# Kernel optimization log

Hardware: AMD Instinct MI355X
Metric: run time of the kernel (lower is better)

The kernel has to match this reference:

```python
import math
import jax, jax.numpy as jnp
import numpy as np

LEVELS = 4          # wavelet_levels
PRUNE = 0.05        # wavelet_packet_prune_ratio
EPS = 1e-6
SQRT2 = math.sqrt(2.0)


def _haar_split(c):
    n = c.shape[-1]
    if n % 2 != 0:
        c = jnp.concatenate([c, jnp.zeros(c.shape[:-1] + (1,), c.dtype)], axis=-1)
    even, odd = c[..., 0::2], c[..., 1::2]
    return (even + odd) / SQRT2, (even - odd) / SQRT2, n


def _haar_merge(low, high, orig):
    even = (low + high) / SQRT2
    odd = (low - high) / SQRT2
    out = jnp.stack([even, odd], axis=-1).reshape(*low.shape[:-1], low.shape[-1] * 2)
    return out[..., :orig]


def _coherence(c, gpu):
    unit = c / jnp.maximum(jnp.abs(c), EPS)
    return jnp.clip(jnp.abs(jnp.mean(unit * jnp.conj(gpu), axis=-1, keepdims=True)), 0.0, 1.0)


def _cost(c, gpu):
    # gauge-aware packet cost: Shannon entropy of energy distribution + (1 - coherence)
    if c.shape[-1] <= 1:
        return jnp.float32(0.0)
    e = jnp.square(jnp.abs(c))
    p = jnp.maximum(e / jnp.maximum(e.sum(-1, keepdims=True), EPS), EPS)
    ent = -(p * jnp.log(p)).sum(-1)
    coh = _coherence(c, gpu)[..., 0]
    return jax.lax.stop_gradient(jnp.mean(ent + (1.0 - coh)))


def _band_center(path):
    if not path:
        return 0.0
    idx = 0
    for b in path:
        idx = (idx << 1) | b
    return (idx + 0.5) / (2 ** len(path))


def _leaf_gain(c, path, depth, gpu, Wp, bp, Wo, bo, lfg, sigma, hfg, cutoff):
    mag = jnp.maximum(jnp.abs(c), EPS)
    phase = jnp.arctan2(c.imag, c.real) / math.pi
    nle = jnp.broadcast_to(
        jnp.log(jnp.maximum(jnp.mean(jnp.square(jnp.abs(c)), -1, keepdims=True), EPS)), mag.shape)
    dn = jnp.full(mag.shape, depth / max(1, LEVELS), mag.dtype)
    bcv = _band_center(path)
    bc = jnp.full(mag.shape, bcv, mag.dtype)
    coh = jnp.broadcast_to(_coherence(c, gpu), mag.shape)
    pos = jnp.broadcast_to(jnp.linspace(0.0, 1.0, c.shape[-1], dtype=mag.dtype), mag.shape)
    feats = jnp.stack([jnp.log(mag), phase, nle, dn, bc, coh, pos], axis=-1)  # [..., n, 7]
    gd = jax.nn.silu(feats @ Wp.T + bp) @ Wo.T + bo                            # [..., n, 2]
    dm = 0.25 * jnp.tanh(gd[..., 0])
    dp = 0.5 * math.pi * jnp.tanh(gd[..., 1])
    lbb = 1.0 + lfg * jnp.exp(-(bcv * bcv) / jnp.square(sigma))
    hbd = hfg + (1.0 - hfg) * jax.nn.sigmoid((cutoff - bcv) / sigma)
    gm = lbb * hbd * (1.0 + lfg * coh) * (hfg + (1.0 - hfg) * coh) * jnp.exp(dm)
    return jax.lax.complex(gm * jnp.cos(dp), gm * jnp.sin(dp))  # torch.polar


def _filter_leaf(c, path, depth, total_e, gpu, params):
    Wp, bp, Wo, bo, lfg, sigma, hfg, cutoff = params
    node_e = jax.lax.stop_gradient(jnp.square(jnp.abs(c)).sum())
    filtered = c * _leaf_gain(c, path, depth, gpu, Wp, bp, Wo, bo, lfg, sigma, hfg, cutoff)
    coh_v = jax.lax.stop_gradient(jnp.mean(_coherence(c, gpu)))
    # spectral subtraction
    fm = jnp.abs(filtered)
    nf = jnp.median(fm, axis=-1, keepdims=True)
    damping = hfg + (1.0 - hfg) * jax.nn.sigmoid((cutoff - _band_center(path)) / sigma)
    den = jax.nn.relu(fm - (1.0 - damping) * nf)
    filtered = den * (filtered / jnp.maximum(fm, EPS))
    # prune low-energy / low-coherence leaves
    prune = jnp.logical_or(node_e / total_e < PRUNE, coh_v < PRUNE)
    return jnp.where(prune, filtered * jnp.square(hfg), filtered)


def _apply_node(c, depth, path, total_e, gpu, params):
    cost = _cost(c, gpu)
    leaf = _filter_leaf(c, path, depth, total_e, gpu, params)
    if depth >= LEVELS or c.shape[-1] <= 1:
        return leaf, cost
    low, high, orig = _haar_split(c)
    lr, lc = _apply_node(low, depth + 1, path + (0,), total_e, gpu, params)
    hr, hc = _apply_node(high, depth + 1, path + (1,), total_e, gpu, params)
    merged = _haar_merge(lr, hr, orig)
    child_cost = lc + hc
    # best-basis selection (wavelet_packet_best_basis=True)
    out = jnp.where(child_cost < cost, merged, leaf)
    return out, jnp.minimum(child_cost, cost)


def setup_inputs() -> dict:
    key = jax.random.key(0)
    ks = jax.random.split(key, 3)
    B, R, N = 8, 64, 8192
    x = jax.random.normal(ks[0], (B, R, N), jnp.float32)
    Wp = jax.random.normal(ks[1], (12, 7), jnp.float32) * math.sqrt(2.0 / 19.0)  # xavier-ish
    bp = jnp.zeros((12,), jnp.float32)
    Wo = jax.random.normal(ks[2], (2, 12), jnp.float32) * 0.1
    bo = jnp.zeros((2,), jnp.float32)
    return {"x": x, "Wp": Wp, "bp": bp, "Wo": Wo, "bo": bo,
            "lfg": jnp.float32(0.5), "sigma": jnp.float32(0.3),
            "hfg": jnp.float32(0.7), "cutoff": jnp.float32(0.25)}


def reference(x, Wp, bp, Wo, bo, lfg, sigma, hfg, cutoff):
    n = x.shape[-1]
    spec = jnp.fft.fft(x)  # complex64 [B, R, N]
    # _fft_filter spectral gating
    r2 = jnp.square(jnp.fft.fftfreq(n).astype(x.dtype))
    lfb = 1.0 + lfg * jnp.exp(-r2 / jnp.square(sigma))
    radius = jnp.sqrt(r2 + 1e-12)
    gate = jax.nn.sigmoid((cutoff - radius) / jnp.maximum(sigma, 0.05))
    spec = spec * (lfb * (hfg + (1.0 - hfg) * gate))
    # global phase unit
    unit = spec / jnp.maximum(jnp.abs(spec), EPS)
    g = jnp.mean(unit, axis=-1, keepdims=True)
    gpu = g / jnp.maximum(jnp.abs(g), EPS)
    total_e = jax.lax.stop_gradient(jnp.square(jnp.abs(spec)).sum())
    params = (Wp, bp, Wo, bo, lfg, sigma, hfg, cutoff)
    out, _ = _apply_node(spec, 0, (), total_e, gpu, params)
    return jnp.fft.ifft(out).real
```

## Files before the change

kernel.cpp:

```cpp
#include <hip/hip_runtime.h>
#include <hip/hip_fp16.h>
#include <math.h>

#define NN      8192
#define LOGN    13
#define ROWS    512
#define NT      512
#define NNODES  31
#define EPSF    1e-6f
#define PRUNEF  0.05f
#define SQRT1_2F 0.70710678118654752f
#define PIF      3.14159265358979323f
#define INV_PIF  0.31830988618379067f
#define HALF_PIF 1.57079632679489662f

typedef unsigned int uint;

__device__ __forceinline__ float fast_rcp(float x){ return __builtin_amdgcn_rcpf(x); }
__device__ __forceinline__ float fast_rsq(float x){ return __builtin_amdgcn_rsqf(x); }

__device__ __forceinline__ float tanh_pade(float y){
    y = fminf(3.f, fmaxf(-3.f, y));
    float y2 = y * y;
    float num = y * fmaf(y2, 10.f, 105.f);
    float den = fmaf(y2, 45.f, fmaf(y2 * y2, 1.f, 105.f));
    return num * fast_rcp(den);
}
__device__ __forceinline__ float silu_pade(float h){
    float y = fminf(3.f, fmaxf(-3.f, 0.5f * h));
    float y2 = y * y;
    float num = y * fmaf(y2, 10.f, 105.f);
    float den = fmaf(y2, 45.f, fmaf(y2 * y2, 1.f, 105.f));
    return 0.5f * h * (1.f + num * fast_rcp(den));
}
__device__ __forceinline__ float exp_small(float z){
    return fmaf(z, fmaf(z, fmaf(z, fmaf(z, 0.041666667f, 0.16666667f), 0.5f), 1.f), 1.f);
}
__device__ __forceinline__ float sin_halfpi(float t){
    float t2 = t * t;
    return t * fmaf(t2, fmaf(t2, fmaf(t2, -4.6817541e-3f, 7.96926262e-2f), -6.45964097e-1f), 1.57079632f);
}
__device__ __forceinline__ float cos_halfpi(float t){
    float t2 = t * t;
    return fmaf(t2, fmaf(t2, fmaf(t2, fmaf(t2, 9.1937e-4f, -2.08634807e-2f), 2.53669508e-1f), -1.23370055f), 1.f);
}

__device__ __forceinline__ float fast_atan2f(float y, float x) {
    float ay = fabsf(y), ax = fabsf(x);
    float mx = fmaxf(ax, ay), mn = fminf(ax, ay);
    float a = (mx > 0.f) ? (mn * fast_rcp(mx)) : 0.f;
    bool big = a > 0.4142135679f;
    float t = big ? ((a - 1.f) * fast_rcp(a + 1.f)) : a;
    float z2 = t * t;
    float p = fmaf(8.05374449538e-2f, z2, -1.38776856032e-1f);
    p = fmaf(p, z2, 1.99777106478e-1f);
    p = fmaf(p, z2, -3.33329491539e-1f);
    float r = fmaf(p * z2, t, t);
    if (big) r += 0.78539816339744831f;
    if (ay > ax) r = 1.57079632679489662f - r;
    if (x < 0.f) r = 3.14159265358979323f - r;
    return copysignf(r, y);
}

__device__ __forceinline__ float2 cmul(float2 a, float2 b){
    return make_float2(a.x*b.x - a.y*b.y, a.x*b.y + a.y*b.x);
}
__device__ __forceinline__ float2 cadd(float2 a, float2 b){ return make_float2(a.x+b.x, a.y+b.y); }
__device__ __forceinline__ float2 csub(float2 a, float2 b){ return make_float2(a.x-b.x, a.y-b.y); }

__device__ __forceinline__ uint pack_h2(float2 v){
    __half2 h = __floats2half2_rn(v.x, v.y);
    return __builtin_bit_cast(uint, h);
}
__device__ __forceinline__ float2 unpack_h2(uint u){
    __half2 h = __builtin_bit_cast(__half2, u);
    return make_float2(__low2float(h), __high2float(h));
}

__device__ __forceinline__ void wave_red8(float* a) {
    #pragma unroll
    for (int m = 32; m >= 1; m >>= 1) {
        #pragma unroll
        for (int q = 0; q < 8; ++q) a[q] += __shfl_xor(a[q], m);
    }
}

template<int DP>
__device__ __forceinline__ void level_split_stats(
    float2 (&v)[16], float* nacc, int tid)
{
    constexpr int ST = 8 >> DP;
    #pragma unroll
    for (int t = 0; t < 16; ++t) {
        if ((t & ST) == 0) {
            float2 a = v[t], b = v[t + ST];
            v[t]      = make_float2((a.x + b.x) * SQRT1_2F, (a.y + b.y) * SQRT1_2F);
            v[t + ST] = make_float2((a.x - b.x) * SQRT1_2F, (a.y - b.y) * SQRT1_2F);
        }
    }
    constexpr int CNT = 16 >> (DP + 1);
    constexpr int NPAIR = 1 << DP;
    constexpr int G0 = (2 << DP) - 1;
    #pragma unroll
    for (int pr = 0; pr < NPAIR; ++pr) {
        float acc[8] = {0,0,0,0,0,0,0,0};
        #pragma unroll
        for (int s = 0; s < CNT; ++s) {
            float2 w = v[(2 * pr) * CNT + s];
            float e = fmaf(w.x, w.x, w.y * w.y);
            acc[0] += e; acc[1] += e * __logf(fmaxf(e, 1e-30f));
            float iv = fminf(fast_rsq(e), 1e6f);
            acc[2] += w.x * iv; acc[3] += w.y * iv;
        }
        #pragma unroll
        for (int s = 0; s < CNT; ++s) {
            float2 w = v[(2 * pr + 1) * CNT + s];
            float e = fmaf(w.x, w.x, w.y * w.y);
            acc[4] += e; acc[5] += e * __logf(fmaxf(e, 1e-30f));
            float iv = fminf(fast_rsq(e), 1e6f);
            acc[6] += w.x * iv; acc[7] += w.y * iv;
        }
        wave_red8(acc);
        if ((tid & 63) == 0) {
            int ga = G0 + 2 * pr, gb = ga + 1;
            atomicAdd(&nacc[(ga - 1) * 4 + 0], acc[0]); atomicAdd(&nacc[(ga - 1) * 4 + 1], acc[1]);
            atomicAdd(&nacc[(ga - 1) * 4 + 2], acc[2]); atomicAdd(&nacc[(ga - 1) * 4 + 3], acc[3]);
            atomicAdd(&nacc[(gb - 1) * 4 + 0], acc[4]); atomicAdd(&nacc[(gb - 1) * 4 + 1], acc[5]);
            atomicAdd(&nacc[(gb - 1) * 4 + 2], acc[6]); atomicAdd(&nacc[(gb - 1) * 4 + 3], acc[7]);
        }
    }
}

__global__ __launch_bounds__(NT, 4) void k_pre(
    const float* __restrict__ x, uint* __restrict__ Lv16,
    float* __restrict__ Se, float* __restrict__ Coh, float* __restrict__ Ent,
    const float* lfg_p, const float* sig_p, const float* hfg_p, const float* cut_p)
{
    __shared__ float2 sh[NN];
    __shared__ float4 wred[8];
    __shared__ float nacc[30 * 4];
    int row = blockIdx.x, tid = threadIdx.x;
    float lfg = *lfg_p, sigma = *sig_p, hfg = *hfg_p, cutoff = *cut_p;

    const float* xr = x + ((size_t)row << LOGN);
    #pragma unroll
    for (int t = 0; t < 16; ++t) {
        int i = tid + (t << 9);
        sh[i] = make_float2(xr[i], 0.f);
    }
    __syncthreads();

    for (int sp = 0; sp < 6; ++sp) {
        int lg = 11 - 2 * sp;
        int Hh = 1 << lg;
        float angf = -PIF / (float)(2 * Hh);
        #pragma unroll 4
        for (int c = 0; c < 4; ++c) {
            int q = tid + (c << 9);
            int j = q & (Hh - 1);
            int p = ((q >> lg) << (lg + 2)) | j;
            float2 a = sh[p], b = sh[p + Hh], cc = sh[p + 2 * Hh], d = sh[p + 3 * Hh];
            float ang = angf * (float)j;
            float s = __sinf(ang), co = __cosf(ang);
            float2 t1 = make_float2(co, s);
            float2 t2 = make_float2(co * co - s * s, 2.f * co * s);
            float2 a1 = cadd(a, cc);
            float2 c1 = cmul(csub(a, cc), t1);
            float2 b1 = cadd(b, d);
            float2 u  = cmul(csub(b, d), t1);
            float2 d1 = make_float2(u.y, -u.x);
            sh[p]          = cadd(a1, b1);
            sh[p + Hh]     = cmul(csub(a1, b1), t2);
            sh[p + 2 * Hh] = cadd(c1, d1);
            sh[p + 3 * Hh] = cmul(csub(c1, d1), t2);
        }
        __syncthreads();
    }
    #pragma unroll 8
    for (int c = 0; c < 8; ++c) {
        int p = (tid + (c << 9)) << 1;
        float2 a = sh[p], b = sh[p + 1];
        sh[p] = cadd(a, b);
        sh[p + 1] = csub(a, b);
    }
    __syncthreads();

    if (tid < 120) nacc[tid] = 0.f;
    float inv_gs = 1.f / fmaxf(sigma, 0.05f);
    float is2 = 1.f / (sigma * sigma);
    float se = 0.f, slg = 0.f, sux = 0.f, suy = 0.f;
    float2 v[16];
    #pragma unroll
    for (int t = 0; t < 16; ++t) {
        int p = tid + (t << 9);
        int k = (int)(__brev((uint)p) >> 19);
        float fk = (k < NN / 2) ? (float)k : (float)(k - NN);
        float f = fk * (1.0f / (float)NN);
        float r2 = f * f;
        float lfb = 1.f + lfg * __expf(-r2 * is2);
        float radius = sqrtf(r2 + 1e-12f);
        float gate = fast_rcp(1.f + __expf(-(cutoff - radius) * inv_gs));
        float mult = lfb * (hfg + (1.f - hfg) * gate);
        float2 c = sh[p];
        c.x *= mult; c.y *= mult;
        v[t] = c;
        float e = fmaf(c.x, c.x, c.y * c.y);
        se += e;
        slg += e * __logf(fmaxf(e, 1e-30f));
        float inv = fminf(fast_rsq(e), 1e6f);
        sux += c.x * inv; suy += c.y * inv;
    }
    #pragma unroll
    for (int m = 32; m >= 1; m >>= 1) {
        se += __shfl_xor(se, m); slg += __shfl_xor(slg, m);
        sux += __shfl_xor(sux, m); suy += __shfl_xor(suy, m);
    }
    if ((tid & 63) == 0) wred[tid >> 6] = make_float4(se, slg, sux, suy);
    __syncthreads();
    if (tid == 0) {
        float4 r = wred[0];
        #pragma unroll
        for (int w = 1; w < 8; ++w) {
            r.x += wred[w].x; r.y += wred[w].y; r.z += wred[w].z; r.w += wred[w].w;
        }
        float gx = r.z / (float)NN, gy = r.w / (float)NN;
        float ga = sqrtf(gx * gx + gy * gy);
        float denom = fmaxf(r.x, EPSF);
        Se[row]  = r.x;
        Ent[row] = __logf(denom) - r.y / denom;
        Coh[row] = fminf(ga, 1.f);
    }

    level_split_stats<0>(v, nacc, tid);
    level_split_stats<1>(v, nacc, tid);
    level_split_stats<2>(v, nacc, tid);
    level_split_stats<3>(v, nacc, tid);
    __syncthreads();
    if (tid < 30) {
        int g = tid + 1;
        float E = nacc[tid * 4 + 0], SL = nacc[tid * 4 + 1];
        float ZX = nacc[tid * 4 + 2], ZY = nacc[tid * 4 + 3];
        float denom = fmaxf(E, EPSF);
        float ent = __logf(denom) - SL / denom;
        int d = 31 - __clz(g + 1);
        float invn = 1.f / (float)(NN >> d);
        float zx = ZX * invn, zy = ZY * invn;
        float ch = fminf(sqrtf(zx * zx + zy * zy), 1.f);
        Se[g * ROWS + row] = E; Coh[g * ROWS + row] = ch; Ent[g * ROWS + row] = ent;
    }

    uint* lrow = Lv16 + ((size_t)row << LOGN);
    #pragma unroll
    for (int t = 0; t < 16; ++t)
        lrow[tid + (t << 9)] = pack_h2(v[t]);
}

__global__ __launch_bounds__(NT) void k_decide(
    const float* __restrict__ Se, const float* __restrict__ Coh, const float* __restrict__ Ent,
    int* __restrict__ fFg, int* __restrict__ fPg)
{
    __shared__ float dtmp[3 * NNODES];
    __shared__ int fF[NNODES], fP[NNODES];
    int tid = threadIdx.x;
    float* dcost = dtmp; float* dne = dtmp + NNODES; float* dcm = dtmp + 2 * NNODES;
    int wid = tid >> 6, lane = tid & 63;
    for (int gn = wid; gn < NNODES; gn += 8) {
        float a = 0.f, b = 0.f, cc = 0.f;
        #pragma unroll
        for (int rr = 0; rr < ROWS / 64; ++rr) {
            int r = lane + (rr << 6);
            float ch = Coh[gn * ROWS + r];
            a += Ent[gn * ROWS + r] + 1.f - ch;
            b += Se[gn * ROWS + r];
            cc += ch;
        }
        #pragma unroll
        for (int m = 32; m >= 1; m >>= 1) {
            a += __shfl_xor(a, m); b += __shfl_xor(b, m); cc += __shfl_xor(cc, m);
        }
        if (lane == 0) { dcost[gn] = a / (float)ROWS; dne[gn] = b; dcm[gn] = cc / (float)ROWS; }
    }
    __syncthreads();
    if (tid == 0) {
        float mc[NNODES]; int sel[NNODES]; int act[NNODES];
        for (int gn = NNODES - 1; gn >= 0; --gn) {
            if (gn >= 15) { mc[gn] = dcost[gn]; sel[gn] = 0; }
            else {
                float chc = mc[2 * gn + 1] + mc[2 * gn + 2];
                sel[gn] = (chc < dcost[gn]) ? 1 : 0;
                mc[gn] = fminf(chc, dcost[gn]);
            }
        }
        float total_e = dne[0];
        act[0] = 1;
        for (int gn = 1; gn < NNODES; ++gn) {
            int p = (gn - 1) >> 1;
            act[gn] = act[p] && sel[p];
        }
        for (int gn = 0; gn < NNODES; ++gn) {
            int isleaf = (gn >= 15);
            fF[gn] = (act[gn] && (isleaf || !sel[gn])) ? 1 : 0;
            fP[gn] = ((dne[gn] / total_e < PRUNEF) || (dcm[gn] < PRUNEF)) ? 1 : 0;
        }
    }
    __syncthreads();
    if (tid < NNODES) { fFg[tid] = fF[tid]; fPg[tid] = fP[tid]; }
}

__device__ __forceinline__ uint key_of(float2 v) {
    return __float_as_uint(fmaf(v.x, v.x, v.y * v.y));
}
__device__ __forceinline__ uint key_at(const float2* sh, int p) { return key_of(sh[p]); }

__device__ __forceinline__ uint2 hist_locate1024(
    const uint* hist, int tid, uint r, uint* wsum, uint* selres)
{
    uint l0 = hist[2 * tid], l1 = hist[2 * tid + 1];
    uint s = l0 + l1;
    uint sc = s;
    #pragma unroll
    for (int o = 1; o < 64; o <<= 1) {
        uint v = __shfl_up(sc, o);
        if ((tid & 63) >= o) sc += v;
    }
    int wid = tid >> 6;
    if ((tid & 63) == 63) wsum[wid] = sc;
    __syncthreads();
    uint wb = 0;
    #pragma unroll
    for (int w = 0; w < 8; ++w) if (w < wid) wb += wsum[w];
    uint c0 = wb + sc - s;
    if (r >= c0 && r < c0 + l0) { selres[0] = 2u * tid;      selres[1] = c0; }
    c0 += l0;
    if (r >= c0 && r < c0 + l1) { selres[0] = 2u * tid + 1u; selres[1] = c0; }
    __syncthreads();
    uint2 res = make_uint2(selres[0], selres[1]);
    __syncthreads();
    return res;
}

template<int EPT>
__device__ __forceinline__ float median_node(
    const float2* sh, int nd, int tid,
    uint* hist, uint* wsum, uint* selres)
{
    uint r1 = (uint)(nd / 2 - 1), r2 = (uint)(nd / 2);
    for (int k = tid; k < 1024; k += NT) hist[k] = 0u;
    __syncthreads();
    #pragma unroll
    for (int c = 0; c < EPT; ++c)
        atomicAdd(&hist[key_at(sh, tid + (c << 9)) >> 21], 1u);
    __syncthreads();
    uint2 A1 = hist_locate1024(hist, tid, r1, wsum, selres);
    uint2 A2 = hist_locate1024(hist, tid, r2, wsum, selres);
    uint va, vb;
    if (A1.x != A2.x) {
        if (tid == 0) { selres[0] = 0u; selres[1] = 0xFFFFFFFFu; }
        __syncthreads();
        #pragma unroll
        for (int c = 0; c < EPT; ++c) {
            uint k = key_at(sh, tid + (c << 9));
            uint b = k >> 21;
            if (b == A1.x) atomicMax(&selres[0], k);
            if (b == A2.x) atomicMin(&selres[1], k);
        }
        __syncthreads();
        va = selres[0]; vb = selres[1];
        __syncthreads();
    } else {
        uint p1 = A1.x;
        for (int k = tid; k < 1024; k += NT) hist[k] = 0u;
        __syncthreads();
        #pragma unroll
        for (int c = 0; c < EPT; ++c) {
            uint k = key_at(sh, tid + (c << 9));
            if ((k >> 21) == p1) atomicAdd(&hist[(k >> 11) & 1023u], 1u);
        }
        __syncthreads();
        uint2 B1 = hist_locate1024(hist, tid, r1 - A1.y, wsum, selres);
        uint2 B2 = hist_locate1024(hist, tid, r2 - A1.y, wsum, selres);
        if (B1.x != B2.x) {
            uint pA = (p1 << 10) | B1.x, pB = (p1 << 10) | B2.x;
            if (tid == 0) { selres[0] = 0u; selres[1] = 0xFFFFFFFFu; }
            __syncthreads();
            #pragma unroll
            for (int c = 0; c < EPT; ++c) {
                uint k = key_at(sh, tid + (c << 9));
                uint b = k >> 11;
                if (b == pA) atomicMax(&selres[0], k);
                if (b == pB) atomicMin(&selres[1], k);
            }
            __syncthreads();
            va = selres[0]; vb = selres[1];
            __syncthreads();
        } else {
            uint pfx = (p1 << 10) | B1.x;
            for (int k = tid; k < 1024; k += NT) hist[k] = 0u;
            __syncthreads();
            #pragma unroll
            for (int c = 0; c < EPT; ++c) {
                uint k = key_at(sh, tid + (c << 9));
                if ((k >> 11) == pfx) atomicAdd(&hist[(k >> 1) & 1023u], 1u);
            }
            __syncthreads();
            uint2 C1 = hist_locate1024(hist, tid, r1 - A1.y - B1.y, wsum, selres);
            uint2 C2 = hist_locate1024(hist, tid, r2 - A1.y - B1.y, wsum, selres);
            va = ((pfx << 10) | C1.x) << 1;
            vb = ((pfx << 10) | C2.x) << 1;
        }
    }
    return 0.5f * (sqrtf(__uint_as_float(va)) + sqrtf(__uint_as_float(vb)));
}

__device__ __forceinline__ float median_root_reg(
    const float2 (&v)[16], int tid, uint* hist, uint* wsum, uint* selres)
{
    const uint r1 = NN / 2 - 1, r2 = NN / 2;
    for (int k = tid; k < 1024; k += NT) hist[k] = 0u;
    __syncthreads();
    #pragma unroll
    for (int t = 0; t < 16; ++t)
        atomicAdd(&hist[key_of(v[t]) >> 21], 1u);
    __syncthreads();
    uint2 A1 = hist_locate1024(hist, tid, r1, wsum, selres);
    uint2 A2 = hist_locate1024(hist, tid, r2, wsum, selres);
    uint va, vb;
    if (A1.x != A2.x) {
        if (tid == 0) { selres[0] = 0u; selres[1] = 0xFFFFFFFFu; }
        __syncthreads();
        #pragma unroll
        for (int t = 0; t < 16; ++t) {
            uint k = key_of(v[t]);
            uint b = k >> 21;
            if (b == A1.x) atomicMax(&selres[0], k);
            if (b == A2.x) atomicMin(&selres[1], k);
        }
        __syncthreads();
        va = selres[0]; vb = selres[1];
        __syncthreads();
    } else {
        uint p1 = A1.x;
        for (int k = tid; k < 1024; k += NT) hist[k] = 0u;
        __syncthreads();
        #pragma unroll
        for (int t = 0; t < 16; ++t) {
            uint k = key_of(v[t]);
            if ((k >> 21) == p1) atomicAdd(&hist[(k >> 11) & 1023u], 1u);
        }
        __syncthreads();
        uint2 B1 = hist_locate1024(hist, tid, r1 - A1.y, wsum, selres);
        uint2 B2 = hist_locate1024(hist, tid, r2 - A1.y, wsum, selres);
        if (B1.x != B2.x) {
            uint pA = (p1 << 10) | B1.x, pB = (p1 << 10) | B2.x;
            if (tid == 0) { selres[0] = 0u; selres[1] = 0xFFFFFFFFu; }
            __syncthreads();
            #pragma unroll
            for (int t = 0; t < 16; ++t) {
                uint k = key_of(v[t]);
                uint b = k >> 11;
                if (b == pA) atomicMax(&selres[0], k);
                if (b == pB) atomicMin(&selres[1], k);
            }
            __syncthreads();
            va = selres[0]; vb = selres[1];
            __syncthreads();
        } else {
            uint pfx = (p1 << 10) | B1.x;
            for (int k = tid; k < 1024; k += NT) hist[k] = 0u;
            __syncthreads();
            #pragma unroll
            for (int t = 0; t < 16; ++t) {
                uint k = key_of(v[t]);
                if ((k >> 11) == pfx) atomicAdd(&hist[(k >> 1) & 1023u], 1u);
            }
            __syncthreads();
            uint2 C1 = hist_locate1024(hist, tid, r1 - A1.y - B1.y, wsum, selres);
            uint2 C2 = hist_locate1024(hist, tid, r2 - A1.y - B1.y, wsum, selres);
            va = ((pfx << 10) | C1.x) << 1;
            vb = ((pfx << 10) | C2.x) << 1;
        }
    }
    return 0.5f * (sqrtf(__uint_as_float(va)) + sqrtf(__uint_as_float(vb)));
}

struct NodeConst {
    float hbd, gbase, hb[12], bo0, bo1;
};
__device__ __forceinline__ NodeConst node_consts(
    int D, int nodes, int n, int g, int ND, int row,
    const float* __restrict__ Wp, const float* __restrict__ bp,
    const float* __restrict__ Wo, const float* __restrict__ bo,
    const float* __restrict__ Se, const float* __restrict__ Coh,
    float lfg, float sigma, float hfg, float cutoff, float& coh_o)
{
    NodeConst nc;
    float bcv = (D == 0) ? 0.f : ((float)n + 0.5f) / (float)nodes;
    float coh = Coh[g * ROWS + row];
    float sev = Se[g * ROWS + row];
    float nle = __logf(fmaxf(sev * (1.f / (float)ND), EPSF));
    float dnv = (float)D * 0.25f;
    float lbb = 1.f + lfg * __expf(-(bcv * bcv) / (sigma * sigma));
    nc.hbd = hfg + (1.f - hfg) * fast_rcp(1.f + __expf(-(cutoff - bcv) / sigma));
    nc.gbase = lbb * nc.hbd * (1.f + lfg * coh) * (hfg + (1.f - hfg) * coh);
    #pragma unroll
    for (int j = 0; j < 12; ++j)
        nc.hb[j] = bp[j] + nle * Wp[j*7+2] + dnv * Wp[j*7+3] + bcv * Wp[j*7+4] + coh * Wp[j*7+5];
    nc.bo0 = bo[0]; nc.bo1 = bo[1];
    coh_o = coh;
    return nc;
}

__device__ __forceinline__ float2 mlp_apply(
    float2 cv, int o, int D, float invnm1, const NodeConst& nc,
    const float* __restrict__ Wp, const float* __restrict__ Wo)
{
    float m2 = fmaf(cv.x, cv.x, cv.y * cv.y);
    float f0 = 0.5f * __logf(fmaxf(m2, 1e-12f));
    float f1 = fast_atan2f(cv.y, cv.x) * INV_PIF;
    int itrue = (int)(__brev((uint)o) >> (19 + D));
    float f6 = (float)itrue * invnm1;
    float acc0 = nc.bo0, acc1 = nc.bo1;
    #pragma unroll
    for (int j = 0; j < 12; ++j) {
        float h = fmaf(f0, Wp[j*7], fmaf(f1, Wp[j*7+1], fmaf(f6, Wp[j*7+6], nc.hb[j])));
        float s = silu_pade(h);
        acc0 = fmaf(s, Wo[j], acc0);
        acc1 = fmaf(s, Wo[12 + j], acc1);
    }
    float gm = nc.gbase * exp_small(0.25f * tanh_pade(acc0));
    float tp = tanh_pade(acc1);
    float spv = sin_halfpi(tp), cpv = cos_halfpi(tp);
    return make_float2(gm * (cv.x * cpv - cv.y * spv),
                       gm * (cv.x * spv + cv.y * cpv));
}

template<int D>
__device__ __forceinline__ void filter_node_sh(
    float2 (&v)[16], int n, int tid, float2* sh,
    const float* __restrict__ Wp, const float* __restrict__ bp,
    const float* __restrict__ Wo, const float* __restrict__ bo,
    const float* __restrict__ Se, const float* __restrict__ Coh,
    const int* __restrict__ fPg, int row,
    uint* hist, uint* wsum, uint* selres,
    float lfg, float sigma, float hfg, float cutoff)
{
    constexpr int CNT = 16 >> D;
    constexpr int ND  = NN >> D;
    constexpr int EPT = ND >> 9;
    int g = (1 << D) - 1 + n;

    #pragma unroll
    for (int t = 0; t < 16; ++t) {
        int k = t - n * CNT;
        if ((unsigned)k < (unsigned)CNT) sh[tid + (k << 9)] = v[t];
    }
    __syncthreads();

    float coh;
    NodeConst nc = node_consts(D, 1 << D, n, g, ND, row, Wp, bp, Wo, bo, Se, Coh,
                               lfg, sigma, hfg, cutoff, coh);
    float invnm1 = 1.f / (float)(ND - 1);

    #pragma unroll
    for (int c = 0; c < EPT; ++c) {
        int o = tid + (c << 9);
        sh[o] = mlp_apply(sh[o], o, D, invnm1, nc, Wp, Wo);
    }
    __syncthreads();

    float nf = median_node<EPT>(sh, ND, tid, hist, wsum, selres);
    float thr = (1.f - nc.hbd) * nf;
    float pf = fPg[g] ? (hfg * hfg) : 1.f;

    #pragma unroll
    for (int c = 0; c < EPT; ++c) {
        int o = tid + (c << 9);
        float2 w = sh[o];
        float fm = sqrtf(fmaf(w.x, w.x, w.y * w.y));
        float den = fmaxf(fm - thr, 0.f);
        float s = den * fast_rcp(fmaxf(fm, EPSF)) * pf;
        sh[o] = make_float2(w.x * s, w.y * s);
    }
    __syncthreads();

    #pragma unroll
    for (int t = 0; t < 16; ++t) {
        int k = t - n * CNT;
        if ((unsigned)k < (unsigned)CNT) v[t] = sh[tid + (k << 9)];
    }
    __syncthreads();
}

__device__ __forceinline__ void filter_root_reg(
    float2 (&v)[16], int tid,
    const float* __restrict__ Wp, const float* __restrict__ bp,
    const float* __restrict__ Wo, const float* __restrict__ bo,
    const float* __restrict__ Se, const float* __restrict__ Coh,
    const int* __restrict__ fPg, int row,
    uint* hist, uint* wsum, uint* selres,
    float lfg, float sigma, float hfg, float cutoff)
{
    float coh;
    NodeConst nc = node_consts(0, 1, 0, 0, NN, row, Wp, bp, Wo, bo, Se, Coh,
                               lfg, sigma, hfg, cutoff, coh);
    float invnm1 = 1.f / (float)(NN - 1);

    #pragma unroll
    for (int t = 0; t < 16; ++t) {
        int o = tid + (t << 9);
        v[t] = mlp_apply(v[t], o, 0, invnm1, nc, Wp, Wo);
    }

    float nf = median_root_reg(v, tid, hist, wsum, selres);
    float thr = (1.f - nc.hbd) * nf;
    float pf = fPg[0] ? (hfg * hfg) : 1.f;

    #pragma unroll
    for (int t = 0; t < 16; ++t) {
        float2 w = v[t];
        float fm = sqrtf(fmaf(w.x, w.x, w.y * w.y));
        float den = fmaxf(fm - thr, 0.f);
        float s = den * fast_rcp(fmaxf(fm, EPSF)) * pf;
        v[t] = make_float2(w.x * s, w.y * s);
    }
}

template<int DT>
__device__ __forceinline__ void merge_reg(float2 (&v)[16]){
    #pragma unroll
    for (int t = 0; t < 16; ++t) {
        if ((t & DT) == 0) {
            float2 lo = v[t], hi = v[t + DT];
            v[t]      = make_float2((lo.x + hi.x) * SQRT1_2F, (lo.y + hi.y) * SQRT1_2F);
            v[t + DT] = make_float2((lo.x - hi.x) * SQRT1_2F, (lo.y - hi.y) * SQRT1_2F);
        }
    }
}

__global__ __launch_bounds__(NT, 4) void k_rest(
    const uint* __restrict__ Lv16,
    const float* __restrict__ Se, const float* __restrict__ Coh,
    const int* __restrict__ fFg, const int* __restrict__ fPg,
    float* __restrict__ out,
    const float* __restrict__ Wp, const float* __restrict__ bp,
    const float* __restrict__ Wo, const float* __restrict__ bo,
    const float* lfg_p, const float* sig_p, const float* hfg_p, const float* cut_p)
{
    __shared__ float2 sh[NN];
    __shared__ __align__(16) uint hist[1024];
    __shared__ uint wsum[8];
    __shared__ uint selres[2];

    int row = blockIdx.x, tid = threadIdx.x;
    float lfg = *lfg_p, sigma = *sig_p, hfg = *hfg_p, cutoff = *cut_p;

    const uint* lr = Lv16 + ((size_t)row << LOGN);
    uint raw[16];
    #pragma unroll
    for (int t = 0; t < 16; ++t) raw[t] = lr[tid + (t << 9)];

    float2 v[16];
    #pragma unroll
    for (int t = 0; t < 16; ++t) v[t] = unpack_h2(raw[t]);

    for (int n = 0; n < 16; ++n)
        if (fFg[15 + n])
            filter_node_sh<4>(v, n, tid, sh, Wp, bp, Wo, bo, Se, Coh, fPg, row, hist, wsum, selres, lfg, sigma, hfg, cutoff);

    merge_reg<1>(v);
    for (int n = 0; n < 8; ++n)
        if (fFg[7 + n])
            filter_node_sh<3>(v, n, tid, sh, Wp, bp, Wo, bo, Se, Coh, fPg, row, hist, wsum, selres, lfg, sigma, hfg, cutoff);
    merge_reg<2>(v);
    for (int n = 0; n < 4; ++n)
        if (fFg[3 + n])
            filter_node_sh<2>(v, n, tid, sh, Wp, bp, Wo, bo, Se, Coh, fPg, row, hist, wsum, selres, lfg, sigma, hfg, cutoff);
    merge_reg<4>(v);
    for (int n = 0; n < 2; ++n)
        if (fFg[1 + n])
            filter_node_sh<1>(v, n, tid, sh, Wp, bp, Wo, bo, Se, Coh, fPg, row, hist, wsum, selres, lfg, sigma, hfg, cutoff);
    merge_reg<8>(v);
    if (fFg[0])
        filter_root_reg(v, tid, Wp, bp, Wo, bo, Se, Coh, fPg, row, hist, wsum, selres, lfg, sigma, hfg, cutoff);

    #pragma unroll
    for (int t = 0; t < 16; ++t) sh[tid + (t << 9)] = v[t];
    __syncthreads();

    for (int sp = 0; sp < 6; ++sp) {
        int h = 1 << (2 * sp);
        float angf = PIF / (float)(2 * h);
        #pragma unroll 4
        for (int c = 0; c < 4; ++c) {
            int q = tid + (c << 9);
            int jj = q & (h - 1);
            int p0 = ((q >> (2 * sp)) << (2 * sp + 2)) | jj;
            float ang = angf * (float)jj;
            float s2 = __sinf(ang), c2 = __cosf(ang);
            float2 t2 = make_float2(c2, s2);
            float2 t1 = make_float2(c2 * c2 - s2 * s2, 2.f * c2 * s2);
            float2 a = sh[p0], b = sh[p0 + h], cc = sh[p0 + 2 * h], d = sh[p0 + 3 * h];
            float2 tb = cmul(t1, b);
            float2 ap = cadd(a, tb), bp2 = csub(a, tb);
            float2 td = cmul(t1, d);
            float2 cp = cadd(cc, td), dp2 = csub(cc, td);
            float2 tc = cmul(t2, cp);
            float2 u  = cmul(t2, dp2);
            float2 iB = make_float2(-u.y, u.x);
            sh[p0]         = cadd(ap, tc);
            sh[p0 + h]     = cadd(bp2, iB);
            sh[p0 + 2 * h] = csub(ap, tc);
            sh[p0 + 3 * h] = csub(bp2, iB);
        }
        __syncthreads();
    }
    {
        float angf = PIF / 4096.f;
        #pragma unroll 8
        for (int c = 0; c < 8; ++c) {
            int p = tid + (c << 9);
            float ang = angf * (float)p;
            float s = __sinf(ang), co = __cosf(ang);
            float2 a = sh[p], b = sh[p + 4096];
            float2 tb = cmul(make_float2(co, s), b);
            sh[p] = cadd(a, tb);
            sh[p + 4096] = csub(a, tb);
        }
        __syncthreads();
    }
    float* orow = out + ((size_t)row << LOGN);
    #pragma unroll
    for (int t = 0; t < 16; ++t) {
        int i = tid + (t << 9);
        orow[i] = sh[i].x * (1.0f / (float)NN);
    }
}

extern "C" void kernel_launch(void* const* d_in, const int* in_sizes, int n_in,
                              void* d_out, int out_size, void* d_ws, size_t ws_size,
                              hipStream_t stream) {
    const float* x   = (const float*)d_in[0];
    const float* Wp  = (const float*)d_in[1];
    const float* bp  = (const float*)d_in[2];
    const float* Wo  = (const float*)d_in[3];
    const float* bo  = (const float*)d_in[4];
    const float* lfg = (const float*)d_in[5];
    const float* sig = (const float*)d_in[6];
    const float* hfg = (const float*)d_in[7];
    const float* cut = (const float*)d_in[8];
    float* out = (float*)d_out;

    size_t LVB = (size_t)ROWS * NN * sizeof(uint);
    char* ws = (char*)d_ws;
    uint*   Lv16 = (uint*)ws;
    float*  Se   = (float*)(ws + LVB);
    float*  Coh  = Se  + (size_t)NNODES * ROWS;
    float*  Ent  = Coh + (size_t)NNODES * ROWS;
    int*    fFg  = (int*)(Ent + (size_t)NNODES * ROWS);
    int*    fPg  = fFg + NNODES;
    size_t need = (size_t)((char*)(fPg + NNODES) - ws);
    if (ws_size < need) return;

    dim3 b(NT);
    k_pre   <<<dim3(ROWS), b, 0, stream>>>(x, Lv16, Se, Coh, Ent, lfg, sig, hfg, cut);
    k_decide<<<dim3(1),    b, 0, stream>>>(Se, Coh, Ent, fFg, fPg);
    k_rest  <<<dim3(ROWS), b, 0, stream>>>(Lv16, Se, Coh, fFg, fPg, out, Wp, bp, Wo, bo, lfg, sig, hfg, cut);
}
```

Measured before the change: 131.8 us.

## Do first/last FFT stages in registers and hoist twiddles out of stage loops

The forward FFT now does its first four radix-2 stages (stride 4096 down to 512) in registers on the loaded input before writing to shared memory. The inverse FFT does its last four stages in registers before the global store. This removes several shared-memory passes and barriers from each transform. The remaining radix-4 stages are templated with compile-time strides and compute one twiddle per thread per stage instead of one per butterfly. This adds register pressure under the 4-blocks-per-SM launch bound and changes the twiddle numerics slightly, since several twiddles are built by repeated complex multiplication.

```diff
diff --git a/kernel.cpp b/kernel.cpp
--- a/kernel.cpp
+++ b/kernel.cpp
@@ -85,50 +85,64 @@
     }
 }
 
-template<int DP>
-__device__ __forceinline__ void level_split_stats(
-    float2 (&v)[16], float* nacc, int tid)
-{
-    constexpr int ST = 8 >> DP;
-    #pragma unroll
-    for (int t = 0; t < 16; ++t) {
-        if ((t & ST) == 0) {
-            float2 a = v[t], b = v[t + ST];
-            v[t]      = make_float2((a.x + b.x) * SQRT1_2F, (a.y + b.y) * SQRT1_2F);
-            v[t + ST] = make_float2((a.x - b.x) * SQRT1_2F, (a.y - b.y) * SQRT1_2F);
-        }
-    }
-    constexpr int CNT = 16 >> (DP + 1);
-    constexpr int NPAIR = 1 << DP;
-    constexpr int G0 = (2 << DP) - 1;
-    #pragma unroll
-    for (int pr = 0; pr < NPAIR; ++pr) {
-        float acc[8] = {0,0,0,0,0,0,0,0};
-        #pragma unroll
-        for (int s = 0; s < CNT; ++s) {
-            float2 w = v[(2 * pr) * CNT + s];
-            float e = fmaf(w.x, w.x, w.y * w.y);
-            acc[0] += e; acc[1] += e * __logf(fmaxf(e, 1e-30f));
-            float iv = fminf(fast_rsq(e), 1e6f);
-            acc[2] += w.x * iv; acc[3] += w.y * iv;
-        }
-        #pragma unroll
-        for (int s = 0; s < CNT; ++s) {
-            float2 w = v[(2 * pr + 1) * CNT + s];
-            float e = fmaf(w.x, w.x, w.y * w.y);
-            acc[4] += e; acc[5] += e * __logf(fmaxf(e, 1e-30f));
-            float iv = fminf(fast_rsq(e), 1e6f);
-            acc[6] += w.x * iv; acc[7] += w.y * iv;
-        }
-        wave_red8(acc);
-        if ((tid & 63) == 0) {
-            int ga = G0 + 2 * pr, gb = ga + 1;
-            atomicAdd(&nacc[(ga - 1) * 4 + 0], acc[0]); atomicAdd(&nacc[(ga - 1) * 4 + 1], acc[1]);
-            atomicAdd(&nacc[(ga - 1) * 4 + 2], acc[2]); atomicAdd(&nacc[(ga - 1) * 4 + 3], acc[3]);
-            atomicAdd(&nacc[(gb - 1) * 4 + 0], acc[4]); atomicAdd(&nacc[(gb - 1) * 4 + 1], acc[5]);
-            atomicAdd(&nacc[(gb - 1) * 4 + 2], acc[6]); atomicAdd(&nacc[(gb - 1) * 4 + 3], acc[7]);
-        }
-    }
+#define C8C 0.92387953251f
+#define S8C 0.38268343236f
+#define C4C 0.70710678119f
+
+template<int HH, int LG>
+__device__ __forceinline__ void fwd_r4_stage(float2* sh, int tid) {
+    int j = tid & (HH - 1);
+    float ang = (-PIF / (2.0f * (float)HH)) * (float)j;
+    float s = __sinf(ang), co = __cosf(ang);
+    float2 t1 = make_float2(co, s);
+    float2 t2 = make_float2(co * co - s * s, 2.f * co * s);
+    int g = tid & 127;
+    int i = ((g >> LG) << (LG + 2)) | (g & (HH - 1));
+    #pragma unroll
+    for (int c = 0; c < 4; ++c) {
+        int lb = (tid + (c << 9)) >> 7;
+        int p = (lb << 9) + i;
+        float2 a = sh[p], b = sh[p + HH], cc = sh[p + 2*HH], d = sh[p + 3*HH];
+        float2 a1 = cadd(a, cc);
+        float2 c1 = cmul(csub(a, cc), t1);
+        float2 b1 = cadd(b, d);
+        float2 u  = cmul(csub(b, d), t1);
+        float2 d1 = make_float2(u.y, -u.x);
+        sh[p]        = cadd(a1, b1);
+        sh[p + HH]   = cmul(csub(a1, b1), t2);
+        sh[p + 2*HH] = cadd(c1, d1);
+        sh[p + 3*HH] = cmul(csub(c1, d1), t2);
+    }
+    __syncthreads();
+}
+
+template<int H, int LG>
+__device__ __forceinline__ void inv_r4_stage(float2* sh, int tid) {
+    int jj = tid & (H - 1);
+    float ang = (PIF / (2.0f * (float)H)) * (float)jj;
+    float s2 = __sinf(ang), c2 = __cosf(ang);
+    float2 t2 = make_float2(c2, s2);
+    float2 t1 = make_float2(c2 * c2 - s2 * s2, 2.f * c2 * s2);
+    int g = tid & 127;
+    int i = ((g >> LG) << (LG + 2)) | (g & (H - 1));
+    #pragma unroll
+    for (int c = 0; c < 4; ++c) {
+        int lb = (tid + (c << 9)) >> 7;
+        int p0 = (lb << 9) + i;
+        float2 a = sh[p0], b = sh[p0 + H], cc = sh[p0 + 2*H], d = sh[p0 + 3*H];
+        float2 tb = cmul(t1, b);
+        float2 ap = cadd(a, tb), bp2 = csub(a, tb);
+        float2 td = cmul(t1, d);
+        float2 cp = cadd(cc, td), dp2 = csub(cc, td);
+        float2 tc = cmul(t2, cp);
+        float2 u  = cmul(t2, dp2);
+        float2 iB = make_float2(-u.y, u.x);
+        sh[p0]       = cadd(ap, tc);
+        sh[p0 + H]   = cadd(bp2, iB);
+        sh[p0 + 2*H] = csub(ap, tc);
+        sh[p0 + 3*H] = csub(bp2, iB);
+    }
+    __syncthreads();
 }
 
 __global__ __launch_bounds__(NT, 4) void k_pre(
@@ -143,40 +157,60 @@
     float lfg = *lfg_p, sigma = *sig_p, hfg = *hfg_p, cutoff = *cut_p;
 
     const float* xr = x + ((size_t)row << LOGN);
-    #pragma unroll
-    for (int t = 0; t < 16; ++t) {
-        int i = tid + (t << 9);
-        sh[i] = make_float2(xr[i], 0.f);
-    }
-    __syncthreads();
-
-    for (int sp = 0; sp < 6; ++sp) {
-        int lg = 11 - 2 * sp;
-        int Hh = 1 << lg;
-        float angf = -PIF / (float)(2 * Hh);
-        #pragma unroll 4
-        for (int c = 0; c < 4; ++c) {
-            int q = tid + (c << 9);
-            int j = q & (Hh - 1);
-            int p = ((q >> lg) << (lg + 2)) | j;
-            float2 a = sh[p], b = sh[p + Hh], cc = sh[p + 2 * Hh], d = sh[p + 3 * Hh];
-            float ang = angf * (float)j;
-            float s = __sinf(ang), co = __cosf(ang);
-            float2 t1 = make_float2(co, s);
-            float2 t2 = make_float2(co * co - s * s, 2.f * co * s);
-            float2 a1 = cadd(a, cc);
-            float2 c1 = cmul(csub(a, cc), t1);
-            float2 b1 = cadd(b, d);
-            float2 u  = cmul(csub(b, d), t1);
-            float2 d1 = make_float2(u.y, -u.x);
-            sh[p]          = cadd(a1, b1);
-            sh[p + Hh]     = cmul(csub(a1, b1), t2);
-            sh[p + 2 * Hh] = cadd(c1, d1);
-            sh[p + 3 * Hh] = cmul(csub(c1, d1), t2);
-        }
-        __syncthreads();
-    }
-    #pragma unroll 8
+    float2 v[16];
+    #pragma unroll
+    for (int t = 0; t < 16; ++t)
+        v[t] = make_float2(xr[tid + (t << 9)], 0.f);
+
+    {
+        float a0 = -PIF * (1.0f / 4096.0f) * (float)tid;
+        float2 w1 = make_float2(__cosf(a0), __sinf(a0));
+        float2 w2 = cmul(w1, w1);
+        float2 w4 = cmul(w2, w2);
+        float2 w8 = cmul(w4, w4);
+        const float2 K16[8] = {
+            { 1.f, 0.f}, { C8C, -S8C}, { C4C, -C4C}, { S8C, -C8C},
+            { 0.f,-1.f}, {-S8C, -C8C}, {-C4C, -C4C}, {-C8C, -S8C}};
+        #pragma unroll
+        for (int t = 0; t < 8; ++t) {
+            float2 W = cmul(w1, K16[t]);
+            float2 a = v[t], b = v[t + 8];
+            v[t] = cadd(a, b);
+            v[t + 8] = cmul(csub(a, b), W);
+        }
+        const float2 K8a[4] = {{1.f,0.f},{C4C,-C4C},{0.f,-1.f},{-C4C,-C4C}};
+        #pragma unroll
+        for (int t = 0; t < 16; ++t) if (!(t & 4)) {
+            float2 W = cmul(w2, K8a[t & 3]);
+            float2 a = v[t], b = v[t + 4];
+            v[t] = cadd(a, b);
+            v[t + 4] = cmul(csub(a, b), W);
+        }
+        #pragma unroll
+        for (int t = 0; t < 16; ++t) if (!(t & 2)) {
+            float2 W = (t & 1) ? make_float2(w4.y, -w4.x) : w4;
+            float2 a = v[t], b = v[t + 2];
+            v[t] = cadd(a, b);
+            v[t + 2] = cmul(csub(a, b), W);
+        }
+        #pragma unroll
+        for (int t = 0; t < 16; ++t) if (!(t & 1)) {
+            float2 a = v[t], b = v[t + 1];
+            v[t] = cadd(a, b);
+            v[t + 1] = cmul(csub(a, b), w8);
+        }
+    }
+
+    if (tid < 120) nacc[tid] = 0.f;
+
+    #pragma unroll
+    for (int t = 0; t < 16; ++t) sh[tid + (t << 9)] = v[t];
+    __syncthreads();
+    fwd_r4_stage<128, 7>(sh, tid);
+    fwd_r4_stage<32, 5>(sh, tid);
+    fwd_r4_stage<8, 3>(sh, tid);
+    fwd_r4_stage<2, 1>(sh, tid);
+    #pragma unroll
     for (int c = 0; c < 8; ++c) {
         int p = (tid + (c << 9)) << 1;
         float2 a = sh[p], b = sh[p + 1];
@@ -185,11 +219,9 @@
     }
     __syncthreads();
 
-    if (tid < 120) nacc[tid] = 0.f;
     float inv_gs = 1.f / fmaxf(sigma, 0.05f);
     float is2 = 1.f / (sigma * sigma);
     float se = 0.f, slg = 0.f, sux = 0.f, suy = 0.f;
-    float2 v[16];
     #pragma unroll
     for (int t = 0; t < 16; ++t) {
         int p = tid + (t << 9);
@@ -231,10 +263,52 @@
         Coh[row] = fminf(ga, 1.f);
     }
 
-    level_split_stats<0>(v, nacc, tid);
-    level_split_stats<1>(v, nacc, tid);
-    level_split_stats<2>(v, nacc, tid);
-    level_split_stats<3>(v, nacc, tid);
+    #pragma unroll
+    for (int DP = 0; DP < 4; ++DP) {
+        int ST = 8 >> DP;
+        #pragma unroll
+        for (int t = 0; t < 16; ++t) {
+            if ((t & ST) == 0) {
+                float2 a = v[t], b = v[t + ST];
+                v[t]      = make_float2((a.x + b.x) * SQRT1_2F, (a.y + b.y) * SQRT1_2F);
+                v[t + ST] = make_float2((a.x - b.x) * SQRT1_2F, (a.y - b.y) * SQRT1_2F);
+            }
+        }
+        int CNT = 16 >> (DP + 1);
+        int NPAIR = 1 << DP;
+        int G0 = (2 << DP) - 1;
+        #pragma unroll
+        for (int pr = 0; pr < NPAIR; ++pr) {
+            float acc[8] = {0,0,0,0,0,0,0,0};
+            #pragma unroll
+            for (int s = 0; s < 16; ++s) {
+                int k0 = s - (2 * pr) * CNT;
+                if (k0 >= 0 && k0 < CNT) {
+                    float2 w = v[s];
+                    float e = fmaf(w.x, w.x, w.y * w.y);
+                    acc[0] += e; acc[1] += e * __logf(fmaxf(e, 1e-30f));
+                    float iv = fminf(fast_rsq(e), 1e6f);
+                    acc[2] += w.x * iv; acc[3] += w.y * iv;
+                }
+                int k1 = s - (2 * pr + 1) * CNT;
+                if (k1 >= 0 && k1 < CNT) {
+                    float2 w = v[s];
+                    float e = fmaf(w.x, w.x, w.y * w.y);
+                    acc[4] += e; acc[5] += e * __logf(fmaxf(e, 1e-30f));
+                    float iv = fminf(fast_rsq(e), 1e6f);
+                    acc[6] += w.x * iv; acc[7] += w.y * iv;
+                }
+            }
+            wave_red8(acc);
+            if ((tid & 63) == 0) {
+                int ga = G0 + 2 * pr, gb = ga + 1;
+                atomicAdd(&nacc[(ga-1)*4+0], acc[0]); atomicAdd(&nacc[(ga-1)*4+1], acc[1]);
+                atomicAdd(&nacc[(ga-1)*4+2], acc[2]); atomicAdd(&nacc[(ga-1)*4+3], acc[3]);
+                atomicAdd(&nacc[(gb-1)*4+0], acc[4]); atomicAdd(&nacc[(gb-1)*4+1], acc[5]);
+                atomicAdd(&nacc[(gb-1)*4+2], acc[6]); atomicAdd(&nacc[(gb-1)*4+3], acc[7]);
+            }
+        }
+    }
     __syncthreads();
     if (tid < 30) {
         int g = tid + 1;
@@ -491,7 +565,7 @@
     const float* __restrict__ Wp, const float* __restrict__ bp,
     const float* __restrict__ Wo, const float* __restrict__ bo,
     const float* __restrict__ Se, const float* __restrict__ Coh,
-    float lfg, float sigma, float hfg, float cutoff, float& coh_o)
+    float lfg, float sigma, float hfg, float cutoff)
 {
     NodeConst nc;
     float bcv = (D == 0) ? 0.f : ((float)n + 0.5f) / (float)nodes;
@@ -506,7 +580,6 @@
     for (int j = 0; j < 12; ++j)
         nc.hb[j] = bp[j] + nle * Wp[j*7+2] + dnv * Wp[j*7+3] + bcv * Wp[j*7+4] + coh * Wp[j*7+5];
     nc.bo0 = bo[0]; nc.bo1 = bo[1];
-    coh_o = coh;
     return nc;
 }
 
@@ -556,9 +629,8 @@
     }
     __syncthreads();
 
-    float coh;
     NodeConst nc = node_consts(D, 1 << D, n, g, ND, row, Wp, bp, Wo, bo, Se, Coh,
-                               lfg, sigma, hfg, cutoff, coh);
+                               lfg, sigma, hfg, cutoff);
     float invnm1 = 1.f / (float)(ND - 1);
 
     #pragma unroll
@@ -600,9 +672,8 @@
     uint* hist, uint* wsum, uint* selres,
     float lfg, float sigma, float hfg, float cutoff)
 {
-    float coh;
     NodeConst nc = node_consts(0, 1, 0, 0, NN, row, Wp, bp, Wo, bo, Se, Coh,
-                               lfg, sigma, hfg, cutoff, coh);
+                               lfg, sigma, hfg, cutoff);
     float invnm1 = 1.f / (float)(NN - 1);
 
     #pragma unroll
@@ -666,7 +737,6 @@
     for (int n = 0; n < 16; ++n)
         if (fFg[15 + n])
             filter_node_sh<4>(v, n, tid, sh, Wp, bp, Wo, bo, Se, Coh, fPg, row, hist, wsum, selres, lfg, sigma, hfg, cutoff);
-
     merge_reg<1>(v);
     for (int n = 0; n < 8; ++n)
         if (fFg[7 + n])
@@ -687,53 +757,76 @@
     for (int t = 0; t < 16; ++t) sh[tid + (t << 9)] = v[t];
     __syncthreads();
 
-    for (int sp = 0; sp < 6; ++sp) {
-        int h = 1 << (2 * sp);
-        float angf = PIF / (float)(2 * h);
-        #pragma unroll 4
-        for (int c = 0; c < 4; ++c) {
+    inv_r4_stage<1, 0>(sh, tid);
+    inv_r4_stage<4, 2>(sh, tid);
+    inv_r4_stage<16, 4>(sh, tid);
+    inv_r4_stage<64, 6>(sh, tid);
+    {
+        int jj = tid & 255;
+        float ang = (PIF / 256.0f) * (float)jj;
+        float2 W = make_float2(__cosf(ang), __sinf(ang));
+        #pragma unroll
+        for (int c = 0; c < 8; ++c) {
             int q = tid + (c << 9);
-            int jj = q & (h - 1);
-            int p0 = ((q >> (2 * sp)) << (2 * sp + 2)) | jj;
-            float ang = angf * (float)jj;
-            float s2 = __sinf(ang), c2 = __cosf(ang);
-            float2 t2 = make_float2(c2, s2);
-            float2 t1 = make_float2(c2 * c2 - s2 * s2, 2.f * c2 * s2);
-            float2 a = sh[p0], b = sh[p0 + h], cc = sh[p0 + 2 * h], d = sh[p0 + 3 * h];
-            float2 tb = cmul(t1, b);
-            float2 ap = cadd(a, tb), bp2 = csub(a, tb);
-            float2 td = cmul(t1, d);
-            float2 cp = cadd(cc, td), dp2 = csub(cc, td);
-            float2 tc = cmul(t2, cp);
-            float2 u  = cmul(t2, dp2);
-            float2 iB = make_float2(-u.y, u.x);
-            sh[p0]         = cadd(ap, tc);
-            sh[p0 + h]     = cadd(bp2, iB);
-            sh[p0 + 2 * h] = csub(ap, tc);
-            sh[p0 + 3 * h] = csub(bp2, iB);
-        }
-        __syncthreads();
-    }
+            int lb = q >> 8;
+            int p = (lb << 9) + jj;
+            float2 a = sh[p], b = sh[p + 256];
+            float2 tb = cmul(W, b);
+            sh[p] = cadd(a, tb);
+            sh[p + 256] = csub(a, tb);
+        }
+        __syncthreads();
+    }
+
+    #pragma unroll
+    for (int t = 0; t < 16; ++t) v[t] = sh[tid + (t << 9)];
     {
-        float angf = PIF / 4096.f;
-        #pragma unroll 8
-        for (int c = 0; c < 8; ++c) {
-            int p = tid + (c << 9);
-            float ang = angf * (float)p;
-            float s = __sinf(ang), co = __cosf(ang);
-            float2 a = sh[p], b = sh[p + 4096];
-            float2 tb = cmul(make_float2(co, s), b);
-            sh[p] = cadd(a, tb);
-            sh[p + 4096] = csub(a, tb);
-        }
-        __syncthreads();
-    }
+        float a0 = PIF * (1.0f / 4096.0f) * (float)tid;
+        float2 w1 = make_float2(__cosf(a0), __sinf(a0));
+        float2 w2 = cmul(w1, w1);
+        float2 w4 = cmul(w2, w2);
+        float2 w8 = cmul(w4, w4);
+        #pragma unroll
+        for (int t = 0; t < 16; ++t) if (!(t & 1)) {
+            float2 tb = cmul(w8, v[t + 1]);
+            float2 a = v[t];
+            v[t] = cadd(a, tb);
+            v[t + 1] = csub(a, tb);
+        }
+        #pragma unroll
+        for (int t = 0; t < 16; ++t) if (!(t & 2)) {
+            float2 W = (t & 1) ? make_float2(-w4.y, w4.x) : w4;
+            float2 tb = cmul(W, v[t + 2]);
+            float2 a = v[t];
+            v[t] = cadd(a, tb);
+            v[t + 2] = csub(a, tb);
+        }
+        const float2 K8p[4] = {{1.f,0.f},{C4C,C4C},{0.f,1.f},{-C4C,C4C}};
+        #pragma unroll
+        for (int t = 0; t < 16; ++t) if (!(t & 4)) {
+            float2 W = cmul(w2, K8p[t & 3]);
+            float2 tb = cmul(W, v[t + 4]);
+            float2 a = v[t];
+            v[t] = cadd(a, tb);
+            v[t + 4] = csub(a, tb);
+        }
+        const float2 K16p[8] = {
+            { 1.f, 0.f}, { C8C, S8C}, { C4C, C4C}, { S8C, C8C},
+            { 0.f, 1.f}, {-S8C, C8C}, {-C4C, C4C}, {-C8C, S8C}};
+        #pragma unroll
+        for (int t = 0; t < 8; ++t) {
+            float2 W = cmul(w1, K16p[t]);
+            float2 tb = cmul(W, v[t + 8]);
+            float2 a = v[t];
+            v[t] = cadd(a, tb);
+            v[t + 8] = csub(a, tb);
+        }
+    }
+
     float* orow = out + ((size_t)row << LOGN);
     #pragma unroll
-    for (int t = 0; t < 16; ++t) {
-        int i = tid + (t << 9);
-        orow[i] = sh[i].x * (1.0f / (float)NN);
-    }
+    for (int t = 0; t < 16; ++t)
+        orow[tid + (t << 9)] = v[t].x * (1.0f / (float)NN);
 }
 
 extern "C" void kernel_launch(void* const* d_in, const int* in_sizes, int n_in,
```

After: 131.3 us. About the same (-0.4%).
